# Performance work log

Measured on AMD Instinct MI355X. Metric: run time of the kernel, lower is better.

The kernel has to match this reference:

```python
import math
import jax, jax.numpy as jnp
import numpy as np

H = 4
C_HID = 32

def setup_inputs() -> dict:
    key = jax.random.key(0)
    ks = jax.random.split(key, 8)
    B, N, C = 1, 256, 128
    q_x = jax.random.normal(ks[0], (B, N, N, C), dtype=jnp.float32)
    kv_x = jax.random.normal(ks[1], (B, N, N, C), dtype=jnp.float32)
    tri_bias = jax.random.normal(ks[2], (B, 1, H, N, N), dtype=jnp.float32)
    mask_bias = jnp.zeros((B, N, 1, 1, N), dtype=jnp.float32)
    mask = jnp.ones((B, N, N, N), dtype=jnp.float32)
    s = 1.0 / math.sqrt(C)
    Wq = jax.random.normal(ks[3], (C, H * C_HID), dtype=jnp.float32) * s
    Wk = jax.random.normal(ks[4], (C, H * C_HID), dtype=jnp.float32) * s
    Wv = jax.random.normal(ks[5], (C, H * C_HID), dtype=jnp.float32) * s
    Wg = jax.random.normal(ks[6], (C, H * C_HID), dtype=jnp.float32) * s
    Wo = jax.random.normal(ks[7], (H * C_HID, C), dtype=jnp.float32) * s
    return {"q_x": q_x, "kv_x": kv_x, "tri_bias": tri_bias, "mask_bias": mask_bias,
            "mask": mask, "Wq": Wq, "Wk": Wk, "Wv": Wv, "Wg": Wg, "Wo": Wo}

def reference(q_x, kv_x, tri_bias, mask_bias, mask, Wq, Wk, Wv, Wg, Wo):
    # q_x/kv_x: [B, N, Q, C]; mask is unused in the non-kernel path (mask_bias carries it)
    lead = q_x.shape[:-1]  # [B, N, Q]
    def split_heads(t):  # [..., H*C_HID] -> [..., H, L, C_HID]
        t = t.reshape(t.shape[:-1] + (H, C_HID))
        return jnp.swapaxes(t, -2, -3)
    q = split_heads(q_x @ Wq) / math.sqrt(C_HID)   # [B, N, H, Q, C_hid]
    k = split_heads(kv_x @ Wk)                      # [B, N, H, K, C_hid]
    v = split_heads(kv_x @ Wv)                      # [B, N, H, K, C_hid]
    a = jnp.einsum('bnhqc,bnhkc->bnhqk', q, k)
    a = a + mask_bias + tri_bias                    # biases broadcast over [B, N, H, Q, K]
    a = jax.nn.softmax(a, axis=-1)
    o = jnp.einsum('bnhqk,bnhkc->bnhqc', a, v)      # [B, N, H, Q, C_hid]
    o = jnp.swapaxes(o, -2, -3)                     # [B, N, Q, H, C_hid]
    g = jax.nn.sigmoid(q_x @ Wg).reshape(lead + (H, C_HID))
    o = o * g
    o = o.reshape(lead + (H * C_HID,))
    return o @ Wo                                   # [B, N, Q, C]
```

## Files before the change

kernel.cpp:

```cpp
#include <hip/hip_runtime.h>
#include <hip/hip_bf16.h>

#define NDIM 256
#define QDIM 256
#define CDIM 128
#define HH 4
#define DD 32
#define RROWS (NDIM * QDIM)

__device__ __forceinline__ float bf2f(unsigned short u) {
    unsigned int x = ((unsigned int)u) << 16;
    return __uint_as_float(x);
}
__device__ __forceinline__ unsigned short f2bf(float f) {
    unsigned int x = __float_as_uint(f);
    unsigned int lsb = (x >> 16) & 1u;
    x += 0x7fffu + lsb;
    return (unsigned short)(x >> 16);
}

typedef __bf16 bf16x8v __attribute__((ext_vector_type(8)));
typedef float  f32x4v  __attribute__((ext_vector_type(4)));
union frag_u { uint4 u; bf16x8v v; };

__device__ __forceinline__ bf16x8v cvt8(float4 f0, float4 f1) {
    bf16x8v r;
    r[0] = (__bf16)f0.x; r[1] = (__bf16)f0.y; r[2] = (__bf16)f0.z; r[3] = (__bf16)f0.w;
    r[4] = (__bf16)f1.x; r[5] = (__bf16)f1.y; r[6] = (__bf16)f1.z; r[7] = (__bf16)f1.w;
    return r;
}

__global__ __launch_bounds__(256, 1) void prep_weights(
    const float* __restrict__ Wq, const float* __restrict__ Wk,
    const float* __restrict__ Wv, const float* __restrict__ Wg,
    const float* __restrict__ Wo, unsigned short* __restrict__ wt)
{
    __shared__ unsigned short t[16][130];
    const int p  = blockIdx.x >> 3;
    const int ch = blockIdx.x & 7;
    const float* __restrict__ W = (p == 0) ? Wq : (p == 1) ? Wk :
                                  (p == 2) ? Wv : (p == 3) ? Wg : Wo;
    const int tid = threadIdx.x;
    for (int idx = tid; idx < 2048; idx += 256) {
        int k = idx >> 7, n = idx & 127;
        t[k][n] = f2bf(W[(ch * 16 + k) * 128 + n]);
    }
    __syncthreads();
    unsigned short* dst = wt + (size_t)p * 16384;
    for (int idx = tid; idx < 2048; idx += 256) {
        int n = idx >> 4, k = idx & 15;
        dst[n * 128 + ch * 16 + k] = t[k][n];
    }
}

__global__ __launch_bounds__(512, 4) void proj_mfma(
    const float* __restrict__ qx, const float* __restrict__ kvx,
    const unsigned short* __restrict__ wt,
    unsigned short* __restrict__ q_ws, unsigned short* __restrict__ k_ws,
    unsigned short* __restrict__ v_ws, unsigned short* __restrict__ g_ws)
{
    __shared__ unsigned short xl[64 * 128];
    const int tid = threadIdx.x;
    const int pp = blockIdx.y;
    const float* __restrict__ X = pp ? kvx : qx;
    const unsigned short* __restrict__ WtA = wt + (size_t)(pp ? 1 : 0) * 16384;
    const unsigned short* __restrict__ WtB = wt + (size_t)(pp ? 2 : 3) * 16384;

    const int wv   = tid >> 6;
    const int lane = tid & 63;
    const int col  = lane & 15;
    const int quad = lane >> 4;
    const int r0   = blockIdx.x * 64;
    const int n    = r0 >> 8;
    const int q0   = r0 & 255;

    frag_u bA[4], bB[4];
#pragma unroll
    for (int kt = 0; kt < 4; ++kt) {
        size_t boff = (size_t)(wv * 16 + col) * 128 + kt * 32 + quad * 8;
        bA[kt].u = *(const uint4*)(WtA + boff);
        bB[kt].u = *(const uint4*)(WtB + boff);
    }

#pragma unroll
    for (int i = 0; i < 2; ++i) {
        int idx = i * 512 + tid;
        int row = idx >> 4;
        int s   = idx & 15;
        const float* src = X + (size_t)(r0 + row) * 128 + s * 8;
        float4 f0 = *(const float4*)src;
        float4 f1 = *(const float4*)(src + 4);
        frag_u t; t.v = cvt8(f0, f1);
        *(uint4*)&xl[row * 128 + ((s ^ (row & 7)) << 3)] = t.u;
    }
    __syncthreads();

    f32x4v accA[4], accB[4];
#pragma unroll
    for (int mt = 0; mt < 4; ++mt) {
        accA[mt] = (f32x4v){0.f, 0.f, 0.f, 0.f};
        accB[mt] = (f32x4v){0.f, 0.f, 0.f, 0.f};
    }

    const int x7 = col & 7;
#pragma unroll
    for (int mt = 0; mt < 4; ++mt) {
        frag_u a[4];
#pragma unroll
        for (int kt = 0; kt < 4; ++kt)
            a[kt].u = *(const uint4*)&xl[(mt * 16 + col) * 128 +
                                         ((((kt << 2) | quad) ^ x7) << 3)];
#pragma unroll
        for (int kt = 0; kt < 4; ++kt) {
            accA[mt] = __builtin_amdgcn_mfma_f32_16x16x32_bf16(a[kt].v, bA[kt].v, accA[mt], 0, 0, 0);
            accB[mt] = __builtin_amdgcn_mfma_f32_16x16x32_bf16(a[kt].v, bB[kt].v, accB[mt], 0, 0, 0);
        }
    }

    const int c = wv * 16 + col;
    __syncthreads();

#pragma unroll
    for (int mt = 0; mt < 4; ++mt)
#pragma unroll
        for (int r = 0; r < 4; ++r) {
            int lr = mt * 16 + quad * 4 + r;
            float v = pp ? accA[mt][r] : accA[mt][r] * 0.17677669529663687f;
            xl[lr * 128 + (c ^ ((lr & 7) << 4))] = f2bf(v);
        }
    __syncthreads();
    {
        unsigned short* dst = pp ? k_ws : q_ws;
#pragma unroll
        for (int i = 0; i < 2; ++i) {
            int t = i * 512 + tid;
            int lr = t >> 4;
            int s  = t & 15;
            uint4 v = *(const uint4*)&xl[lr * 128 + ((s ^ ((lr & 7) << 1)) << 3)];
            int h = s >> 2, d0 = (s & 3) << 3;
            *(uint4*)(dst + ((size_t)(n * HH + h) * QDIM + q0 + lr) * DD + d0) = v;
        }
    }
    __syncthreads();

    if (pp == 0) {
#pragma unroll
        for (int mt = 0; mt < 4; ++mt)
#pragma unroll
            for (int r = 0; r < 4; ++r) {
                int lr = mt * 16 + quad * 4 + r;
                float s = 1.0f / (1.0f + __expf(-accB[mt][r]));
                xl[lr * 128 + (c ^ ((lr & 7) << 4))] = f2bf(s);
            }
        __syncthreads();
#pragma unroll
        for (int i = 0; i < 2; ++i) {
            int t = i * 512 + tid;
            int lr = t >> 4;
            int s  = t & 15;
            uint4 v = *(const uint4*)&xl[lr * 128 + ((s ^ ((lr & 7) << 1)) << 3)];
            int h = s >> 2, d0 = (s & 3) << 3;
            *(uint4*)(g_ws + ((size_t)(n * HH + h) * QDIM + q0 + lr) * DD + d0) = v;
        }
    } else {
#pragma unroll
        for (int mt = 0; mt < 4; ++mt)
#pragma unroll
            for (int r = 0; r < 4; ++r) {
                int lr = mt * 16 + quad * 4 + r;
                xl[c * 64 + (lr ^ ((c & 7) << 3))] = f2bf(accB[mt][r]);
            }
        __syncthreads();
#pragma unroll
        for (int i = 0; i < 2; ++i) {
            int t = i * 512 + tid;
            int cc = t >> 3;
            int chunk = t & 7;
            uint4 v = *(const uint4*)&xl[cc * 64 + ((chunk ^ (cc & 7)) << 3)];
            int h = cc >> 5, d = cc & 31;
            *(uint4*)(v_ws + ((size_t)(n * HH + h) * DD + d) * QDIM + q0 + chunk * 8) = v;
        }
    }
}

__global__ __launch_bounds__(256, 4) void attn_kernel(
    const unsigned short* __restrict__ q_ws, const unsigned short* __restrict__ k_ws,
    const unsigned short* __restrict__ v_ws, const unsigned short* __restrict__ g_ws,
    const float* __restrict__ tri, const float* __restrict__ mb,
    unsigned short* __restrict__ o_ws)
{
    __shared__ unsigned short vl[32 * 256];
    __shared__ unsigned short Pl[64 * 72];

    const int tid = threadIdx.x;
    const int b = blockIdx.x;
    const int L = (b & 7) * 512 + (b >> 3);
    const int qc = L & 3;
    const int n  = (L >> 2) & 255;
    const int h  = L >> 10;
    const size_t base  = (size_t)(n * HH + h) * QDIM * DD;
    const size_t vbase = (size_t)(n * HH + h) * DD * QDIM;

    const int wv   = tid >> 6;
    const int lane = tid & 63;
    const int col  = lane & 15;
    const int quad = lane >> 4;
    const int x7   = col & 7;
    const int qg   = qc * 64 + wv * 16 + col;

    frag_u vreg[4];
    const unsigned short* __restrict__ vsrc = v_ws + vbase;
#pragma unroll
    for (int j = 0; j < 4; ++j) {
        int idx = (wv * 4 + j) * 64 + lane;
        int d = idx >> 5, s = idx & 31;
        vreg[j].u = *(const uint4*)(vsrc + d * 256 + ((s ^ (d & 7)) << 3));
    }

    f32x4v bias[16];
#pragma unroll
    for (int mt = 0; mt < 16; ++mt) {
        int k0 = mt * 16 + quad * 4;
        float4 t4 = *(const float4*)&tri[((size_t)(h * 256 + qg)) * 256 + k0];
        float4 m4 = *(const float4*)&mb[n * 256 + k0];
        bias[mt][0] = t4.x + m4.x; bias[mt][1] = t4.y + m4.y;
        bias[mt][2] = t4.z + m4.z; bias[mt][3] = t4.w + m4.w;
    }

    frag_u bq;
    bq.u = *(const uint4*)(q_ws + base + (size_t)qg * DD + quad * 8);

    f32x4v acc[16];
#pragma unroll
    for (int mt = 0; mt < 16; ++mt) {
        frag_u ak;
        ak.u = *(const uint4*)(k_ws + base + (size_t)(mt * 16 + col) * DD + quad * 8);
        acc[mt] = __builtin_amdgcn_mfma_f32_16x16x32_bf16(ak.v, bq.v, bias[mt], 0, 0, 0);
    }

    float mx = -1e30f;
#pragma unroll
    for (int mt = 0; mt < 16; ++mt)
#pragma unroll
        for (int r = 0; r < 4; ++r) mx = fmaxf(mx, acc[mt][r]);
    mx = fmaxf(mx, __shfl_xor(mx, 16));
    mx = fmaxf(mx, __shfl_xor(mx, 32));

    float sum = 0.f;
#pragma unroll
    for (int mt = 0; mt < 16; ++mt)
#pragma unroll
        for (int r = 0; r < 4; ++r) {
            float e = __expf(acc[mt][r] - mx);
            acc[mt][r] = e;
            sum += e;
        }
    sum += __shfl_xor(sum, 16);
    sum += __shfl_xor(sum, 32);
    float inv = 1.0f / sum;

#pragma unroll
    for (int j = 0; j < 4; ++j) {
        int idx = (wv * 4 + j) * 64 + lane;
        *(uint4*)&vl[idx << 3] = vreg[j].u;
    }
    __syncthreads();

    f32x4v o0 = {0.f, 0.f, 0.f, 0.f};
    f32x4v o1 = {0.f, 0.f, 0.f, 0.f};
    const int prow = (wv * 16 + col) * 72;
#pragma unroll
    for (int ch = 0; ch < 4; ++ch) {
#pragma unroll
        for (int mt4 = 0; mt4 < 4; ++mt4) {
            int mt = ch * 4 + mt4;
            ushort4 pk;
            pk.x = f2bf(acc[mt][0]); pk.y = f2bf(acc[mt][1]);
            pk.z = f2bf(acc[mt][2]); pk.w = f2bf(acc[mt][3]);
            *(ushort4*)&Pl[prow + mt4 * 16 + quad * 4] = pk;
        }
#pragma unroll
        for (int kcl = 0; kcl < 2; ++kcl) {
            int kc = ch * 2 + kcl;
            int u0 = ((kc << 2) | quad) ^ x7;
            frag_u ap, b0, b1;
            ap.u = *(const uint4*)&Pl[prow + kcl * 32 + quad * 8];
            b0.u = *(const uint4*)&vl[(col << 8) + (u0 << 3)];
            b1.u = *(const uint4*)&vl[((16 + col) << 8) + (u0 << 3)];
            o0 = __builtin_amdgcn_mfma_f32_16x16x32_bf16(ap.v, b0.v, o0, 0, 0, 0);
            o1 = __builtin_amdgcn_mfma_f32_16x16x32_bf16(ap.v, b1.v, o1, 0, 0, 0);
        }
    }

#pragma unroll
    for (int r = 0; r < 4; ++r) {
        int qi = quad * 4 + r;
        int qglob = qc * 64 + wv * 16 + qi;
        float iv = __shfl(inv, qi);
        size_t ob = (((size_t)(n * HH + h)) * QDIM + qglob) * DD;
        float g0 = bf2f(g_ws[ob + col]);
        o_ws[ob + col] = f2bf(o0[r] * iv * g0);
        float g1 = bf2f(g_ws[ob + 16 + col]);
        o_ws[ob + 16 + col] = f2bf(o1[r] * iv * g1);
    }
}

__global__ __launch_bounds__(512, 6) void outproj_mfma(
    const unsigned short* __restrict__ o_ws, const unsigned short* __restrict__ wt,
    float* __restrict__ out)
{
    __shared__ unsigned short xl[64 * 128];
    const int tid = threadIdx.x;
    const unsigned short* __restrict__ Wt = wt + 4 * 16384;

    const int wv   = tid >> 6;
    const int lane = tid & 63;
    const int col  = lane & 15;
    const int quad = lane >> 4;
    const int r0   = blockIdx.x * 64;
    const int n    = r0 >> 8;
    const int q0   = r0 & 255;

    frag_u bO[4];
#pragma unroll
    for (int kt = 0; kt < 4; ++kt)
        bO[kt].u = *(const uint4*)(Wt + (size_t)(wv * 16 + col) * 128 + kt * 32 + quad * 8);

#pragma unroll
    for (int i = 0; i < 2; ++i) {
        int idx = i * 512 + tid;
        int row = idx >> 4;
        int s   = idx & 15;
        int h   = s >> 2;
        int d   = (s & 3) << 3;
        uint4 v = *(const uint4*)(o_ws +
            ((size_t)(n * HH + h) * QDIM + q0 + row) * DD + d);
        *(uint4*)&xl[row * 128 + ((s ^ (row & 7)) << 3)] = v;
    }
    __syncthreads();

    f32x4v acc[4];
#pragma unroll
    for (int mt = 0; mt < 4; ++mt)
        acc[mt] = (f32x4v){0.f, 0.f, 0.f, 0.f};

    const int x7 = col & 7;
#pragma unroll
    for (int mt = 0; mt < 4; ++mt) {
        frag_u a[4];
#pragma unroll
        for (int kt = 0; kt < 4; ++kt)
            a[kt].u = *(const uint4*)&xl[(mt * 16 + col) * 128 +
                                         ((((kt << 2) | quad) ^ x7) << 3)];
#pragma unroll
        for (int kt = 0; kt < 4; ++kt)
            acc[mt] = __builtin_amdgcn_mfma_f32_16x16x32_bf16(a[kt].v, bO[kt].v, acc[mt], 0, 0, 0);
    }

#pragma unroll
    for (int mt = 0; mt < 4; ++mt)
#pragma unroll
        for (int r = 0; r < 4; ++r) {
            size_t row = r0 + mt * 16 + quad * 4 + r;
            out[row * 128 + wv * 16 + col] = acc[mt][r];
        }
}

extern "C" void kernel_launch(void* const* d_in, const int* in_sizes, int n_in,
                              void* d_out, int out_size, void* d_ws, size_t ws_size,
                              hipStream_t stream) {
    const float* qx  = (const float*)d_in[0];
    const float* kvx = (const float*)d_in[1];
    const float* tri = (const float*)d_in[2];
    const float* mb  = (const float*)d_in[3];
    const float* Wq  = (const float*)d_in[5];
    const float* Wk  = (const float*)d_in[6];
    const float* Wv  = (const float*)d_in[7];
    const float* Wg  = (const float*)d_in[8];
    const float* Wo  = (const float*)d_in[9];
    float* out = (float*)d_out;

    unsigned short* ws = (unsigned short*)d_ws;
    const size_t RC = (size_t)RROWS * 128;
    unsigned short* q_ws = ws;
    unsigned short* k_ws = ws + RC;
    unsigned short* v_ws = ws + 2 * RC;
    unsigned short* g_ws = ws + 3 * RC;
    unsigned short* o_ws = ws + 4 * RC;
    unsigned short* wt   = ws + 5 * RC;

    prep_weights<<<dim3(40), 256, 0, stream>>>(Wq, Wk, Wv, Wg, Wo, wt);
    proj_mfma<<<dim3(RROWS / 64, 2), 512, 0, stream>>>(
        qx, kvx, wt, q_ws, k_ws, v_ws, g_ws);
    attn_kernel<<<dim3(4096), 256, 0, stream>>>(
        q_ws, k_ws, v_ws, g_ws, tri, mb, o_ws);
    outproj_mfma<<<dim3(RROWS / 64), 512, 0, stream>>>(o_ws, wt, out);
}
```

Before: 239.0 us.

## Make projection and attention kernels loop over query chunks with double-buffered prefetch

Each block of the projection and output-projection kernels now processes a full N slice of four 64-row chunks. It prefetches the next chunk's inputs into registers and writes them to a second LDS buffer while computing the current one. The attention kernel processes all four query chunks per (n,h), loading V into shared memory once and reusing it. This amortizes weight and V loads and overlaps global loads with MFMA work. The cost is far fewer blocks, which reduces parallelism and occupancy across the device.

```diff
diff --git a/kernel.cpp b/kernel.cpp
--- a/kernel.cpp
+++ b/kernel.cpp
@@ -59,7 +59,7 @@
     unsigned short* __restrict__ q_ws, unsigned short* __restrict__ k_ws,
     unsigned short* __restrict__ v_ws, unsigned short* __restrict__ g_ws)
 {
-    __shared__ unsigned short xl[64 * 128];
+    __shared__ unsigned short xb[2][64 * 128];
     const int tid = threadIdx.x;
     const int pp = blockIdx.y;
     const float* __restrict__ X = pp ? kvx : qx;
@@ -70,9 +70,12 @@
     const int lane = tid & 63;
     const int col  = lane & 15;
     const int quad = lane >> 4;
-    const int r0   = blockIdx.x * 64;
-    const int n    = r0 >> 8;
-    const int q0   = r0 & 255;
+    const int x7   = col & 7;
+    const int n    = blockIdx.x;
+    const int c    = wv * 16 + col;
+
+    const int srow0 = tid >> 4, ss0 = tid & 15;
+    const int srow1 = (512 + tid) >> 4, ss1 = tid & 15;
 
     frag_u bA[4], bB[4];
 #pragma unroll
@@ -82,104 +85,112 @@
         bB[kt].u = *(const uint4*)(WtB + boff);
     }
 
-#pragma unroll
-    for (int i = 0; i < 2; ++i) {
-        int idx = i * 512 + tid;
-        int row = idx >> 4;
-        int s   = idx & 15;
-        const float* src = X + (size_t)(r0 + row) * 128 + s * 8;
-        float4 f0 = *(const float4*)src;
-        float4 f1 = *(const float4*)(src + 4);
-        frag_u t; t.v = cvt8(f0, f1);
-        *(uint4*)&xl[row * 128 + ((s ^ (row & 7)) << 3)] = t.u;
+    {
+        const float* s0 = X + (size_t)(n * 256 + srow0) * 128 + ss0 * 8;
+        const float* s1 = X + (size_t)(n * 256 + srow1) * 128 + ss1 * 8;
+        float4 a0 = *(const float4*)s0, a1 = *(const float4*)(s0 + 4);
+        float4 b0 = *(const float4*)s1, b1 = *(const float4*)(s1 + 4);
+        frag_u t0; t0.v = cvt8(a0, a1);
+        frag_u t1; t1.v = cvt8(b0, b1);
+        *(uint4*)&xb[0][srow0 * 128 + ((ss0 ^ (srow0 & 7)) << 3)] = t0.u;
+        *(uint4*)&xb[0][srow1 * 128 + ((ss1 ^ (srow1 & 7)) << 3)] = t1.u;
     }
     __syncthreads();
 
-    f32x4v accA[4], accB[4];
-#pragma unroll
-    for (int mt = 0; mt < 4; ++mt) {
-        accA[mt] = (f32x4v){0.f, 0.f, 0.f, 0.f};
-        accB[mt] = (f32x4v){0.f, 0.f, 0.f, 0.f};
-    }
-
-    const int x7 = col & 7;
-#pragma unroll
-    for (int mt = 0; mt < 4; ++mt) {
-        frag_u a[4];
-#pragma unroll
-        for (int kt = 0; kt < 4; ++kt)
-            a[kt].u = *(const uint4*)&xl[(mt * 16 + col) * 128 +
-                                         ((((kt << 2) | quad) ^ x7) << 3)];
-#pragma unroll
-        for (int kt = 0; kt < 4; ++kt) {
-            accA[mt] = __builtin_amdgcn_mfma_f32_16x16x32_bf16(a[kt].v, bA[kt].v, accA[mt], 0, 0, 0);
-            accB[mt] = __builtin_amdgcn_mfma_f32_16x16x32_bf16(a[kt].v, bB[kt].v, accB[mt], 0, 0, 0);
-        }
-    }
-
-    const int c = wv * 16 + col;
-    __syncthreads();
-
-#pragma unroll
-    for (int mt = 0; mt < 4; ++mt)
-#pragma unroll
-        for (int r = 0; r < 4; ++r) {
-            int lr = mt * 16 + quad * 4 + r;
-            float v = pp ? accA[mt][r] : accA[mt][r] * 0.17677669529663687f;
-            xl[lr * 128 + (c ^ ((lr & 7) << 4))] = f2bf(v);
-        }
-    __syncthreads();
-    {
-        unsigned short* dst = pp ? k_ws : q_ws;
-#pragma unroll
-        for (int i = 0; i < 2; ++i) {
-            int t = i * 512 + tid;
-            int lr = t >> 4;
-            int s  = t & 15;
-            uint4 v = *(const uint4*)&xl[lr * 128 + ((s ^ ((lr & 7) << 1)) << 3)];
-            int h = s >> 2, d0 = (s & 3) << 3;
-            *(uint4*)(dst + ((size_t)(n * HH + h) * QDIM + q0 + lr) * DD + d0) = v;
-        }
-    }
-    __syncthreads();
-
-    if (pp == 0) {
+#pragma unroll
+    for (int it = 0; it < 4; ++it) {
+        const int cur = it & 1;
+        const int q0  = it * 64;
+
+        float4 fA0, fA1, fB0, fB1;
+        if (it < 3) {
+            const float* s0 = X + (size_t)(n * 256 + q0 + 64 + srow0) * 128 + ss0 * 8;
+            const float* s1 = X + (size_t)(n * 256 + q0 + 64 + srow1) * 128 + ss1 * 8;
+            fA0 = *(const float4*)s0; fA1 = *(const float4*)(s0 + 4);
+            fB0 = *(const float4*)s1; fB1 = *(const float4*)(s1 + 4);
+        }
+
+        f32x4v accA[4], accB[4];
+#pragma unroll
+        for (int mt = 0; mt < 4; ++mt) {
+            accA[mt] = (f32x4v){0.f, 0.f, 0.f, 0.f};
+            accB[mt] = (f32x4v){0.f, 0.f, 0.f, 0.f};
+        }
+#pragma unroll
+        for (int mt = 0; mt < 4; ++mt) {
+            frag_u a[4];
+#pragma unroll
+            for (int kt = 0; kt < 4; ++kt)
+                a[kt].u = *(const uint4*)&xb[cur][(mt * 16 + col) * 128 +
+                                                  ((((kt << 2) | quad) ^ x7) << 3)];
+#pragma unroll
+            for (int kt = 0; kt < 4; ++kt) {
+                accA[mt] = __builtin_amdgcn_mfma_f32_16x16x32_bf16(a[kt].v, bA[kt].v, accA[mt], 0, 0, 0);
+                accB[mt] = __builtin_amdgcn_mfma_f32_16x16x32_bf16(a[kt].v, bB[kt].v, accB[mt], 0, 0, 0);
+            }
+        }
+        __syncthreads();
+
 #pragma unroll
         for (int mt = 0; mt < 4; ++mt)
 #pragma unroll
             for (int r = 0; r < 4; ++r) {
                 int lr = mt * 16 + quad * 4 + r;
-                float s = 1.0f / (1.0f + __expf(-accB[mt][r]));
-                xl[lr * 128 + (c ^ ((lr & 7) << 4))] = f2bf(s);
-            }
-        __syncthreads();
-#pragma unroll
-        for (int i = 0; i < 2; ++i) {
-            int t = i * 512 + tid;
-            int lr = t >> 4;
-            int s  = t & 15;
-            uint4 v = *(const uint4*)&xl[lr * 128 + ((s ^ ((lr & 7) << 1)) << 3)];
-            int h = s >> 2, d0 = (s & 3) << 3;
-            *(uint4*)(g_ws + ((size_t)(n * HH + h) * QDIM + q0 + lr) * DD + d0) = v;
-        }
-    } else {
-#pragma unroll
-        for (int mt = 0; mt < 4; ++mt)
-#pragma unroll
-            for (int r = 0; r < 4; ++r) {
-                int lr = mt * 16 + quad * 4 + r;
-                xl[c * 64 + (lr ^ ((c & 7) << 3))] = f2bf(accB[mt][r]);
-            }
-        __syncthreads();
-#pragma unroll
-        for (int i = 0; i < 2; ++i) {
-            int t = i * 512 + tid;
-            int cc = t >> 3;
-            int chunk = t & 7;
-            uint4 v = *(const uint4*)&xl[cc * 64 + ((chunk ^ (cc & 7)) << 3)];
-            int h = cc >> 5, d = cc & 31;
-            *(uint4*)(v_ws + ((size_t)(n * HH + h) * DD + d) * QDIM + q0 + chunk * 8) = v;
-        }
+                float v = pp ? accA[mt][r] : accA[mt][r] * 0.17677669529663687f;
+                xb[cur][lr * 128 + (c ^ ((lr & 7) << 4))] = f2bf(v);
+            }
+        __syncthreads();
+        {
+            unsigned short* dst = pp ? k_ws : q_ws;
+            int lr0 = tid >> 4, s0 = tid & 15;
+            int lr1 = (512 + tid) >> 4, s1 = tid & 15;
+            uint4 v0 = *(const uint4*)&xb[cur][lr0 * 128 + ((s0 ^ ((lr0 & 7) << 1)) << 3)];
+            uint4 v1 = *(const uint4*)&xb[cur][lr1 * 128 + ((s1 ^ ((lr1 & 7) << 1)) << 3)];
+            *(uint4*)(dst + ((size_t)(n * HH + (s0 >> 2)) * QDIM + q0 + lr0) * DD + ((s0 & 3) << 3)) = v0;
+            *(uint4*)(dst + ((size_t)(n * HH + (s1 >> 2)) * QDIM + q0 + lr1) * DD + ((s1 & 3) << 3)) = v1;
+        }
+        __syncthreads();
+
+        if (pp == 0) {
+#pragma unroll
+            for (int mt = 0; mt < 4; ++mt)
+#pragma unroll
+                for (int r = 0; r < 4; ++r) {
+                    int lr = mt * 16 + quad * 4 + r;
+                    float s = 1.0f / (1.0f + __expf(-accB[mt][r]));
+                    xb[cur][lr * 128 + (c ^ ((lr & 7) << 4))] = f2bf(s);
+                }
+            __syncthreads();
+            int lr0 = tid >> 4, s0 = tid & 15;
+            int lr1 = (512 + tid) >> 4, s1 = tid & 15;
+            uint4 v0 = *(const uint4*)&xb[cur][lr0 * 128 + ((s0 ^ ((lr0 & 7) << 1)) << 3)];
+            uint4 v1 = *(const uint4*)&xb[cur][lr1 * 128 + ((s1 ^ ((lr1 & 7) << 1)) << 3)];
+            *(uint4*)(g_ws + ((size_t)(n * HH + (s0 >> 2)) * QDIM + q0 + lr0) * DD + ((s0 & 3) << 3)) = v0;
+            *(uint4*)(g_ws + ((size_t)(n * HH + (s1 >> 2)) * QDIM + q0 + lr1) * DD + ((s1 & 3) << 3)) = v1;
+        } else {
+#pragma unroll
+            for (int mt = 0; mt < 4; ++mt)
+#pragma unroll
+                for (int r = 0; r < 4; ++r) {
+                    int lr = mt * 16 + quad * 4 + r;
+                    xb[cur][c * 64 + (lr ^ ((c & 7) << 3))] = f2bf(accB[mt][r]);
+                }
+            __syncthreads();
+            int cc0 = tid >> 3, ch0 = tid & 7;
+            int cc1 = (512 + tid) >> 3, ch1 = tid & 7;
+            uint4 v0 = *(const uint4*)&xb[cur][cc0 * 64 + ((ch0 ^ (cc0 & 7)) << 3)];
+            uint4 v1 = *(const uint4*)&xb[cur][cc1 * 64 + ((ch1 ^ (cc1 & 7)) << 3)];
+            *(uint4*)(v_ws + ((size_t)(n * HH + (cc0 >> 5)) * DD + (cc0 & 31)) * QDIM + q0 + ch0 * 8) = v0;
+            *(uint4*)(v_ws + ((size_t)(n * HH + (cc1 >> 5)) * DD + (cc1 & 31)) * QDIM + q0 + ch1 * 8) = v1;
+        }
+
+        if (it < 3) {
+            frag_u t0; t0.v = cvt8(fA0, fA1);
+            frag_u t1; t1.v = cvt8(fB0, fB1);
+            *(uint4*)&xb[cur ^ 1][srow0 * 128 + ((ss0 ^ (srow0 & 7)) << 3)] = t0.u;
+            *(uint4*)&xb[cur ^ 1][srow1 * 128 + ((ss1 ^ (srow1 & 7)) << 3)] = t1.u;
+        }
+        __syncthreads();
     }
 }
 
@@ -194,10 +205,9 @@
 
     const int tid = threadIdx.x;
     const int b = blockIdx.x;
-    const int L = (b & 7) * 512 + (b >> 3);
-    const int qc = L & 3;
-    const int n  = (L >> 2) & 255;
-    const int h  = L >> 10;
+    const int L = (b & 7) * 128 + (b >> 3);
+    const int h = L >> 8;
+    const int n = L & 255;
     const size_t base  = (size_t)(n * HH + h) * QDIM * DD;
     const size_t vbase = (size_t)(n * HH + h) * DD * QDIM;
 
@@ -206,110 +216,115 @@
     const int col  = lane & 15;
     const int quad = lane >> 4;
     const int x7   = col & 7;
-    const int qg   = qc * 64 + wv * 16 + col;
-
-    frag_u vreg[4];
-    const unsigned short* __restrict__ vsrc = v_ws + vbase;
-#pragma unroll
-    for (int j = 0; j < 4; ++j) {
-        int idx = (wv * 4 + j) * 64 + lane;
-        int d = idx >> 5, s = idx & 31;
-        vreg[j].u = *(const uint4*)(vsrc + d * 256 + ((s ^ (d & 7)) << 3));
-    }
-
-    f32x4v bias[16];
-#pragma unroll
-    for (int mt = 0; mt < 16; ++mt) {
-        int k0 = mt * 16 + quad * 4;
-        float4 t4 = *(const float4*)&tri[((size_t)(h * 256 + qg)) * 256 + k0];
-        float4 m4 = *(const float4*)&mb[n * 256 + k0];
-        bias[mt][0] = t4.x + m4.x; bias[mt][1] = t4.y + m4.y;
-        bias[mt][2] = t4.z + m4.z; bias[mt][3] = t4.w + m4.w;
-    }
-
-    frag_u bq;
-    bq.u = *(const uint4*)(q_ws + base + (size_t)qg * DD + quad * 8);
-
-    f32x4v acc[16];
-#pragma unroll
-    for (int mt = 0; mt < 16; ++mt) {
-        frag_u ak;
-        ak.u = *(const uint4*)(k_ws + base + (size_t)(mt * 16 + col) * DD + quad * 8);
-        acc[mt] = __builtin_amdgcn_mfma_f32_16x16x32_bf16(ak.v, bq.v, bias[mt], 0, 0, 0);
-    }
-
-    float mx = -1e30f;
-#pragma unroll
-    for (int mt = 0; mt < 16; ++mt)
-#pragma unroll
-        for (int r = 0; r < 4; ++r) mx = fmaxf(mx, acc[mt][r]);
-    mx = fmaxf(mx, __shfl_xor(mx, 16));
-    mx = fmaxf(mx, __shfl_xor(mx, 32));
-
-    float sum = 0.f;
-#pragma unroll
-    for (int mt = 0; mt < 16; ++mt)
+
+    {
+        const unsigned short* __restrict__ vsrc = v_ws + vbase;
+        frag_u vreg[4];
+#pragma unroll
+        for (int j = 0; j < 4; ++j) {
+            int idx = (wv * 4 + j) * 64 + lane;
+            int d = idx >> 5, s = idx & 31;
+            vreg[j].u = *(const uint4*)(vsrc + d * 256 + ((s ^ (d & 7)) << 3));
+        }
+#pragma unroll
+        for (int j = 0; j < 4; ++j) {
+            int idx = (wv * 4 + j) * 64 + lane;
+            *(uint4*)&vl[idx << 3] = vreg[j].u;
+        }
+        __syncthreads();
+    }
+
+    const int prow = (wv * 16 + col) * 72;
+
+    for (int qc = 0; qc < 4; ++qc) {
+        const int qg = qc * 64 + wv * 16 + col;
+
+        f32x4v bias[16];
+#pragma unroll
+        for (int mt = 0; mt < 16; ++mt) {
+            int k0 = mt * 16 + quad * 4;
+            float4 t4 = *(const float4*)&tri[((size_t)(h * 256 + qg)) * 256 + k0];
+            float4 m4 = *(const float4*)&mb[n * 256 + k0];
+            bias[mt][0] = t4.x + m4.x; bias[mt][1] = t4.y + m4.y;
+            bias[mt][2] = t4.z + m4.z; bias[mt][3] = t4.w + m4.w;
+        }
+
+        frag_u bq;
+        bq.u = *(const uint4*)(q_ws + base + (size_t)qg * DD + quad * 8);
+
+        f32x4v acc[16];
+#pragma unroll
+        for (int mt = 0; mt < 16; ++mt) {
+            frag_u ak;
+            ak.u = *(const uint4*)(k_ws + base + (size_t)(mt * 16 + col) * DD + quad * 8);
+            acc[mt] = __builtin_amdgcn_mfma_f32_16x16x32_bf16(ak.v, bq.v, bias[mt], 0, 0, 0);
+        }
+
+        float mx = -1e30f;
+#pragma unroll
+        for (int mt = 0; mt < 16; ++mt)
+#pragma unroll
+            for (int r = 0; r < 4; ++r) mx = fmaxf(mx, acc[mt][r]);
+        mx = fmaxf(mx, __shfl_xor(mx, 16));
+        mx = fmaxf(mx, __shfl_xor(mx, 32));
+
+        float sum = 0.f;
+#pragma unroll
+        for (int mt = 0; mt < 16; ++mt)
+#pragma unroll
+            for (int r = 0; r < 4; ++r) {
+                float e = __expf(acc[mt][r] - mx);
+                acc[mt][r] = e;
+                sum += e;
+            }
+        sum += __shfl_xor(sum, 16);
+        sum += __shfl_xor(sum, 32);
+        float inv = 1.0f / sum;
+
+        f32x4v o0 = {0.f, 0.f, 0.f, 0.f};
+        f32x4v o1 = {0.f, 0.f, 0.f, 0.f};
+#pragma unroll
+        for (int ch = 0; ch < 4; ++ch) {
+#pragma unroll
+            for (int mt4 = 0; mt4 < 4; ++mt4) {
+                int mt = ch * 4 + mt4;
+                ushort4 pk;
+                pk.x = f2bf(acc[mt][0]); pk.y = f2bf(acc[mt][1]);
+                pk.z = f2bf(acc[mt][2]); pk.w = f2bf(acc[mt][3]);
+                *(ushort4*)&Pl[prow + mt4 * 16 + quad * 4] = pk;
+            }
+#pragma unroll
+            for (int kcl = 0; kcl < 2; ++kcl) {
+                int kc = ch * 2 + kcl;
+                int u0 = ((kc << 2) | quad) ^ x7;
+                frag_u ap, b0, b1;
+                ap.u = *(const uint4*)&Pl[prow + kcl * 32 + quad * 8];
+                b0.u = *(const uint4*)&vl[(col << 8) + (u0 << 3)];
+                b1.u = *(const uint4*)&vl[((16 + col) << 8) + (u0 << 3)];
+                o0 = __builtin_amdgcn_mfma_f32_16x16x32_bf16(ap.v, b0.v, o0, 0, 0, 0);
+                o1 = __builtin_amdgcn_mfma_f32_16x16x32_bf16(ap.v, b1.v, o1, 0, 0, 0);
+            }
+        }
+
 #pragma unroll
         for (int r = 0; r < 4; ++r) {
-            float e = __expf(acc[mt][r] - mx);
-            acc[mt][r] = e;
-            sum += e;
-        }
-    sum += __shfl_xor(sum, 16);
-    sum += __shfl_xor(sum, 32);
-    float inv = 1.0f / sum;
-
-#pragma unroll
-    for (int j = 0; j < 4; ++j) {
-        int idx = (wv * 4 + j) * 64 + lane;
-        *(uint4*)&vl[idx << 3] = vreg[j].u;
-    }
-    __syncthreads();
-
-    f32x4v o0 = {0.f, 0.f, 0.f, 0.f};
-    f32x4v o1 = {0.f, 0.f, 0.f, 0.f};
-    const int prow = (wv * 16 + col) * 72;
-#pragma unroll
-    for (int ch = 0; ch < 4; ++ch) {
-#pragma unroll
-        for (int mt4 = 0; mt4 < 4; ++mt4) {
-            int mt = ch * 4 + mt4;
-            ushort4 pk;
-            pk.x = f2bf(acc[mt][0]); pk.y = f2bf(acc[mt][1]);
-            pk.z = f2bf(acc[mt][2]); pk.w = f2bf(acc[mt][3]);
-            *(ushort4*)&Pl[prow + mt4 * 16 + quad * 4] = pk;
-        }
-#pragma unroll
-        for (int kcl = 0; kcl < 2; ++kcl) {
-            int kc = ch * 2 + kcl;
-            int u0 = ((kc << 2) | quad) ^ x7;
-            frag_u ap, b0, b1;
-            ap.u = *(const uint4*)&Pl[prow + kcl * 32 + quad * 8];
-            b0.u = *(const uint4*)&vl[(col << 8) + (u0 << 3)];
-            b1.u = *(const uint4*)&vl[((16 + col) << 8) + (u0 << 3)];
-            o0 = __builtin_amdgcn_mfma_f32_16x16x32_bf16(ap.v, b0.v, o0, 0, 0, 0);
-            o1 = __builtin_amdgcn_mfma_f32_16x16x32_bf16(ap.v, b1.v, o1, 0, 0, 0);
-        }
-    }
-
-#pragma unroll
-    for (int r = 0; r < 4; ++r) {
-        int qi = quad * 4 + r;
-        int qglob = qc * 64 + wv * 16 + qi;
-        float iv = __shfl(inv, qi);
-        size_t ob = (((size_t)(n * HH + h)) * QDIM + qglob) * DD;
-        float g0 = bf2f(g_ws[ob + col]);
-        o_ws[ob + col] = f2bf(o0[r] * iv * g0);
-        float g1 = bf2f(g_ws[ob + 16 + col]);
-        o_ws[ob + 16 + col] = f2bf(o1[r] * iv * g1);
-    }
-}
-
-__global__ __launch_bounds__(512, 6) void outproj_mfma(
+            int qi = quad * 4 + r;
+            int qglob = qc * 64 + wv * 16 + qi;
+            float iv = __shfl(inv, qi);
+            size_t ob = (((size_t)(n * HH + h)) * QDIM + qglob) * DD;
+            float g0 = bf2f(g_ws[ob + col]);
+            o_ws[ob + col] = f2bf(o0[r] * iv * g0);
+            float g1 = bf2f(g_ws[ob + 16 + col]);
+            o_ws[ob + 16 + col] = f2bf(o1[r] * iv * g1);
+        }
+    }
+}
+
+__global__ __launch_bounds__(512, 4) void outproj_mfma(
     const unsigned short* __restrict__ o_ws, const unsigned short* __restrict__ wt,
     float* __restrict__ out)
 {
-    __shared__ unsigned short xl[64 * 128];
+    __shared__ unsigned short xb[2][64 * 128];
     const int tid = threadIdx.x;
     const unsigned short* __restrict__ Wt = wt + 4 * 16384;
 
@@ -317,53 +332,68 @@
     const int lane = tid & 63;
     const int col  = lane & 15;
     const int quad = lane >> 4;
-    const int r0   = blockIdx.x * 64;
-    const int n    = r0 >> 8;
-    const int q0   = r0 & 255;
+    const int x7   = col & 7;
+    const int n    = blockIdx.x;
+
+    const int srow0 = tid >> 4, ss0 = tid & 15;
+    const int srow1 = (512 + tid) >> 4, ss1 = tid & 15;
+    const int sh0 = ss0 >> 2, sd0 = (ss0 & 3) << 3;
+    const int sh1 = ss1 >> 2, sd1 = (ss1 & 3) << 3;
 
     frag_u bO[4];
 #pragma unroll
     for (int kt = 0; kt < 4; ++kt)
         bO[kt].u = *(const uint4*)(Wt + (size_t)(wv * 16 + col) * 128 + kt * 32 + quad * 8);
 
-#pragma unroll
-    for (int i = 0; i < 2; ++i) {
-        int idx = i * 512 + tid;
-        int row = idx >> 4;
-        int s   = idx & 15;
-        int h   = s >> 2;
-        int d   = (s & 3) << 3;
-        uint4 v = *(const uint4*)(o_ws +
-            ((size_t)(n * HH + h) * QDIM + q0 + row) * DD + d);
-        *(uint4*)&xl[row * 128 + ((s ^ (row & 7)) << 3)] = v;
+    {
+        uint4 v0 = *(const uint4*)(o_ws + ((size_t)(n * HH + sh0) * QDIM + srow0) * DD + sd0);
+        uint4 v1 = *(const uint4*)(o_ws + ((size_t)(n * HH + sh1) * QDIM + srow1) * DD + sd1);
+        *(uint4*)&xb[0][srow0 * 128 + ((ss0 ^ (srow0 & 7)) << 3)] = v0;
+        *(uint4*)&xb[0][srow1 * 128 + ((ss1 ^ (srow1 & 7)) << 3)] = v1;
     }
     __syncthreads();
 
-    f32x4v acc[4];
-#pragma unroll
-    for (int mt = 0; mt < 4; ++mt)
-        acc[mt] = (f32x4v){0.f, 0.f, 0.f, 0.f};
-
-    const int x7 = col & 7;
-#pragma unroll
-    for (int mt = 0; mt < 4; ++mt) {
-        frag_u a[4];
-#pragma unroll
-        for (int kt = 0; kt < 4; ++kt)
-            a[kt].u = *(const uint4*)&xl[(mt * 16 + col) * 128 +
-                                         ((((kt << 2) | quad) ^ x7) << 3)];
-#pragma unroll
-        for (int kt = 0; kt < 4; ++kt)
-            acc[mt] = __builtin_amdgcn_mfma_f32_16x16x32_bf16(a[kt].v, bO[kt].v, acc[mt], 0, 0, 0);
-    }
-
-#pragma unroll
-    for (int mt = 0; mt < 4; ++mt)
-#pragma unroll
-        for (int r = 0; r < 4; ++r) {
-            size_t row = r0 + mt * 16 + quad * 4 + r;
-            out[row * 128 + wv * 16 + col] = acc[mt][r];
-        }
+#pragma unroll
+    for (int it = 0; it < 4; ++it) {
+        const int cur = it & 1;
+        const int q0  = it * 64;
+
+        uint4 vn0, vn1;
+        if (it < 3) {
+            vn0 = *(const uint4*)(o_ws + ((size_t)(n * HH + sh0) * QDIM + q0 + 64 + srow0) * DD + sd0);
+            vn1 = *(const uint4*)(o_ws + ((size_t)(n * HH + sh1) * QDIM + q0 + 64 + srow1) * DD + sd1);
+        }
+
+        f32x4v acc[4];
+#pragma unroll
+        for (int mt = 0; mt < 4; ++mt)
+            acc[mt] = (f32x4v){0.f, 0.f, 0.f, 0.f};
+#pragma unroll
+        for (int mt = 0; mt < 4; ++mt) {
+            frag_u a[4];
+#pragma unroll
+            for (int kt = 0; kt < 4; ++kt)
+                a[kt].u = *(const uint4*)&xb[cur][(mt * 16 + col) * 128 +
+                                                  ((((kt << 2) | quad) ^ x7) << 3)];
+#pragma unroll
+            for (int kt = 0; kt < 4; ++kt)
+                acc[mt] = __builtin_amdgcn_mfma_f32_16x16x32_bf16(a[kt].v, bO[kt].v, acc[mt], 0, 0, 0);
+        }
+
+#pragma unroll
+        for (int mt = 0; mt < 4; ++mt)
+#pragma unroll
+            for (int r = 0; r < 4; ++r) {
+                size_t row = (size_t)n * 256 + q0 + mt * 16 + quad * 4 + r;
+                out[row * 128 + wv * 16 + col] = acc[mt][r];
+            }
+
+        if (it < 3) {
+            *(uint4*)&xb[cur ^ 1][srow0 * 128 + ((ss0 ^ (srow0 & 7)) << 3)] = vn0;
+            *(uint4*)&xb[cur ^ 1][srow1 * 128 + ((ss1 ^ (srow1 & 7)) << 3)] = vn1;
+        }
+        __syncthreads();
+    }
 }
 
 extern "C" void kernel_launch(void* const* d_in, const int* in_sizes, int n_in,
@@ -390,9 +420,9 @@
     unsigned short* wt   = ws + 5 * RC;
 
     prep_weights<<<dim3(40), 256, 0, stream>>>(Wq, Wk, Wv, Wg, Wo, wt);
-    proj_mfma<<<dim3(RROWS / 64, 2), 512, 0, stream>>>(
+    proj_mfma<<<dim3(NDIM, 2), 512, 0, stream>>>(
         qx, kvx, wt, q_ws, k_ws, v_ws, g_ws);
-    attn_kernel<<<dim3(4096), 256, 0, stream>>>(
+    attn_kernel<<<dim3(NDIM * HH), 256, 0, stream>>>(
         q_ws, k_ws, v_ws, g_ws, tri, mb, o_ws);
-    outproj_mfma<<<dim3(RROWS / 64), 512, 0, stream>>>(o_ws, wt, out);
-}
+    outproj_mfma<<<dim3(NDIM), 512, 0, stream>>>(o_ws, wt, out);
+}
```

New measurement: 359.8 us. 1.51x slower.
